# Kernel optimization log

Hardware: AMD Instinct MI355X
Metric: run time of the kernel (lower is better)

## Reference

```python
import jax, jax.numpy as jnp
import numpy as np

B, N, C, H = 2, 512, 64, 8

def setup_inputs() -> dict:
    key = jax.random.key(0)
    k1, k2, k3, k4, k5 = jax.random.split(key, 5)
    query = jax.random.normal(k1, (B, N, N, C), dtype=jnp.float32)
    key_t = jax.random.normal(k2, (B, N, N, C), dtype=jnp.float32)
    roi_mask = jax.random.uniform(k3, (B, N, N), dtype=jnp.float32)
    W = jax.random.normal(k4, (H, 2 * C), dtype=jnp.float32) * (1.0 / np.sqrt(2 * C))
    b = jax.random.normal(k5, (H,), dtype=jnp.float32) * 0.01
    return {"query": query, "key": key_t, "roi_mask": roi_mask, "W": W, "b": b}

def reference(query, key, roi_mask, W, b):
    # ft = cat(query, key) along feature dim -> [B, N, N, 2C]
    # small GEMM: scores [B, N, N, H]; split the matmul to avoid materializing concat
    Wq, Wk = W[:, :C], W[:, C:]  # [H, C] each
    attn = jnp.einsum('bmnc,hc->bmnh', query, Wq) \
         + jnp.einsum('bmnc,hc->bmnh', key, Wk) + b
    attn = jnp.exp(attn) * roi_mask[:, :, :, None]
    attn_sum = attn.sum(axis=2)  # [B, N, H]
    return attn / attn_sum[:, :, None, :]
```

## Files before the change

### kernel.cpp

```cpp
#include <hip/hip_runtime.h>
#include <math.h>

constexpr int BDIM    = 256;
constexpr int TILE    = 256;
constexpr int NDIM    = 512;
constexpr int CDIM    = 64;
constexpr int HDIM    = 8;
constexpr int CHALF   = 32;
constexpr int LSTRIDE = CHALF + 1;

__global__ __launch_bounds__(BDIM)
void mha_kernel(const float* __restrict__ q,
                const float* __restrict__ kk,
                const float* __restrict__ mask,
                const float* __restrict__ W,
                const float* __restrict__ bias,
                float* __restrict__ out)
{
    __shared__ float tile_lds[TILE * LSTRIDE];
    __shared__ float red[4 * HDIM];
    __shared__ float rsum_lds[HDIM];

    const int bm = blockIdx.x;
    const int t  = threadIdx.x;

    const float* qrow = q  + (size_t)bm * NDIM * CDIM;
    const float* krow = kk + (size_t)bm * NDIM * CDIM;

    float val[2][HDIM];
    float psum[HDIM];
#pragma unroll
    for (int h = 0; h < HDIM; ++h) psum[h] = 0.0f;

#pragma unroll
    for (int tl = 0; tl < 2; ++tl) {
        const int n0 = tl * TILE;
        float acc[HDIM];
#pragma unroll
        for (int h = 0; h < HDIM; ++h) acc[h] = 0.0f;

        for (int ph = 0; ph < 4; ++ph) {
            const float* srcbase = (ph < 2) ? qrow : krow;
            const float* src = srcbase + (size_t)n0 * CDIM + (ph & 1) * CHALF;

            __syncthreads();
#pragma unroll
            for (int i = 0; i < 8; ++i) {
                int f4 = t + i * BDIM;
                int n  = f4 >> 3;
                int c4 = (f4 & 7) << 2;
                float4 v = *(const float4*)(src + n * CDIM + c4);
                float* d = &tile_lds[n * LSTRIDE + c4];
                d[0] = v.x; d[1] = v.y; d[2] = v.z; d[3] = v.w;
            }
            __syncthreads();

            float x[CHALF];
            const float* xs = &tile_lds[t * LSTRIDE];
#pragma unroll
            for (int c = 0; c < CHALF; ++c) x[c] = xs[c];

            const float* wp = W + ph * CHALF;
#pragma unroll
            for (int h = 0; h < HDIM; ++h) {
                float a = acc[h];
#pragma unroll
                for (int c = 0; c < CHALF; ++c)
                    a = fmaf(x[c], wp[h * 2 * CDIM + c], a);
                acc[h] = a;
            }
        }

        const float mval = mask[bm * NDIM + n0 + t];
#pragma unroll
        for (int h = 0; h < HDIM; ++h) {
            float v = __expf(acc[h] + bias[h]) * mval;
            val[tl][h] = v;
            psum[h] += v;
        }
    }

#pragma unroll
    for (int h = 0; h < HDIM; ++h) {
        float s = psum[h];
#pragma unroll
        for (int off = 32; off >= 1; off >>= 1)
            s += __shfl_xor(s, off, 64);
        psum[h] = s;
    }
    const int lane = t & 63;
    const int wid  = t >> 6;
    if (lane == 0) {
#pragma unroll
        for (int h = 0; h < HDIM; ++h) red[wid * HDIM + h] = psum[h];
    }
    __syncthreads();
    if (t < HDIM) {
        float s = red[t] + red[HDIM + t] + red[2 * HDIM + t] + red[3 * HDIM + t];
        rsum_lds[t] = 1.0f / s;
    }
    __syncthreads();

    float rs[HDIM];
#pragma unroll
    for (int h = 0; h < HDIM; ++h) rs[h] = rsum_lds[h];

    float* orow = out + (size_t)bm * NDIM * HDIM;
#pragma unroll
    for (int tl = 0; tl < 2; ++tl) {
        const int n = tl * TILE + t;
        float4 lo = make_float4(val[tl][0] * rs[0], val[tl][1] * rs[1],
                                val[tl][2] * rs[2], val[tl][3] * rs[3]);
        float4 hi = make_float4(val[tl][4] * rs[4], val[tl][5] * rs[5],
                                val[tl][6] * rs[6], val[tl][7] * rs[7]);
        float4* op = (float4*)(orow + (size_t)n * HDIM);
        op[0] = lo;
        op[1] = hi;
    }
}

extern "C" void kernel_launch(void* const* d_in, const int* in_sizes, int n_in,
                              void* d_out, int out_size, void* d_ws, size_t ws_size,
                              hipStream_t stream) {
    const float* q    = (const float*)d_in[0];
    const float* k    = (const float*)d_in[1];
    const float* mask = (const float*)d_in[2];
    const float* W    = (const float*)d_in[3];
    const float* b    = (const float*)d_in[4];
    float* out = (float*)d_out;

    hipLaunchKernelGGL(mha_kernel, dim3(2 * NDIM), dim3(BDIM), 0, stream,
                       q, k, mask, W, b, out);
}
```

Before: 298.1 us.

## Load query/key rows directly into registers instead of staging through LDS

Drops the shared-memory tile staging and its barriers. Each thread now reads its own 64-float query and key rows with float4 global loads into registers and computes all eight head dot products, and launch bounds request four blocks per CU. This removes LDS traffic and syncs, but each thread's loads now stride 256 bytes apart, so global access is uncoalesced per instruction, and the 64-float register array raises register pressure.

```diff
diff --git a/kernel.cpp b/kernel.cpp
--- a/kernel.cpp
+++ b/kernel.cpp
@@ -1,15 +1,12 @@
 #include <hip/hip_runtime.h>
 #include <math.h>
 
-constexpr int BDIM    = 256;
-constexpr int TILE    = 256;
-constexpr int NDIM    = 512;
-constexpr int CDIM    = 64;
-constexpr int HDIM    = 8;
-constexpr int CHALF   = 32;
-constexpr int LSTRIDE = CHALF + 1;
+constexpr int BDIM = 256;
+constexpr int NDIM = 512;
+constexpr int CDIM = 64;
+constexpr int HDIM = 8;
 
-__global__ __launch_bounds__(BDIM)
+__global__ __launch_bounds__(BDIM, 4)
 void mha_kernel(const float* __restrict__ q,
                 const float* __restrict__ kk,
                 const float* __restrict__ mask,
@@ -17,7 +14,6 @@
                 const float* __restrict__ bias,
                 float* __restrict__ out)
 {
-    __shared__ float tile_lds[TILE * LSTRIDE];
     __shared__ float red[4 * HDIM];
     __shared__ float rsum_lds[HDIM];
 
@@ -34,44 +30,53 @@
 
 #pragma unroll
     for (int tl = 0; tl < 2; ++tl) {
-        const int n0 = tl * TILE;
+        const int n = tl * BDIM + t;
+
         float acc[HDIM];
 #pragma unroll
         for (int h = 0; h < HDIM; ++h) acc[h] = 0.0f;
 
-        for (int ph = 0; ph < 4; ++ph) {
-            const float* srcbase = (ph < 2) ? qrow : krow;
-            const float* src = srcbase + (size_t)n0 * CDIM + (ph & 1) * CHALF;
-
-            __syncthreads();
+        {
+            const float4* qp = (const float4*)(qrow + (size_t)n * CDIM);
+            float x[CDIM];
 #pragma unroll
-            for (int i = 0; i < 8; ++i) {
-                int f4 = t + i * BDIM;
-                int n  = f4 >> 3;
-                int c4 = (f4 & 7) << 2;
-                float4 v = *(const float4*)(src + n * CDIM + c4);
-                float* d = &tile_lds[n * LSTRIDE + c4];
-                d[0] = v.x; d[1] = v.y; d[2] = v.z; d[3] = v.w;
+            for (int j = 0; j < 16; ++j) {
+                float4 v = qp[j];
+                x[4 * j + 0] = v.x; x[4 * j + 1] = v.y;
+                x[4 * j + 2] = v.z; x[4 * j + 3] = v.w;
             }
-            __syncthreads();
-
-            float x[CHALF];
-            const float* xs = &tile_lds[t * LSTRIDE];
-#pragma unroll
-            for (int c = 0; c < CHALF; ++c) x[c] = xs[c];
-
-            const float* wp = W + ph * CHALF;
 #pragma unroll
             for (int h = 0; h < HDIM; ++h) {
+                const float* wq = W + h * 2 * CDIM;
                 float a = acc[h];
 #pragma unroll
-                for (int c = 0; c < CHALF; ++c)
-                    a = fmaf(x[c], wp[h * 2 * CDIM + c], a);
+                for (int c = 0; c < CDIM; ++c)
+                    a = fmaf(x[c], wq[c], a);
                 acc[h] = a;
             }
         }
 
-        const float mval = mask[bm * NDIM + n0 + t];
+        {
+            const float4* kp = (const float4*)(krow + (size_t)n * CDIM);
+            float x[CDIM];
+#pragma unroll
+            for (int j = 0; j < 16; ++j) {
+                float4 v = kp[j];
+                x[4 * j + 0] = v.x; x[4 * j + 1] = v.y;
+                x[4 * j + 2] = v.z; x[4 * j + 3] = v.w;
+            }
+#pragma unroll
+            for (int h = 0; h < HDIM; ++h) {
+                const float* wk = W + h * 2 * CDIM + CDIM;
+                float a = acc[h];
+#pragma unroll
+                for (int c = 0; c < CDIM; ++c)
+                    a = fmaf(x[c], wk[c], a);
+                acc[h] = a;
+            }
+        }
+
+        const float mval = mask[bm * NDIM + n];
 #pragma unroll
         for (int h = 0; h < HDIM; ++h) {
             float v = __expf(acc[h] + bias[h]) * mval;
@@ -108,7 +113,7 @@
     float* orow = out + (size_t)bm * NDIM * HDIM;
 #pragma unroll
     for (int tl = 0; tl < 2; ++tl) {
-        const int n = tl * TILE + t;
+        const int n = tl * BDIM + t;
         float4 lo = make_float4(val[tl][0] * rs[0], val[tl][1] * rs[1],
                                 val[tl][2] * rs[2], val[tl][3] * rs[3]);
         float4 hi = make_float4(val[tl][4] * rs[4], val[tl][5] * rs[5],
```

Result: no change. 296.6 us (-0.5%).

## Split into chunked projection kernel plus separate normalization kernel

Applied to the files above, without the earlier changes.

Each row of the work now goes to 16 blocks of 32 columns instead of one block. Each block computes the unnormalized exp scores with per-thread float4 loads and a shuffle reduction across 16 lanes, then writes partial sums to the workspace. A second kernel reads the partial sums and rescales the output in place. This removes the LDS staging and transposed reads, and gives far more blocks for parallelism and latency hiding. The cost is a second launch and an extra read and write of the output.

```diff
diff --git a/kernel.cpp b/kernel.cpp
--- a/kernel.cpp
+++ b/kernel.cpp
@@ -1,121 +1,136 @@
 #include <hip/hip_runtime.h>
 #include <math.h>
 
-constexpr int BDIM    = 256;
-constexpr int TILE    = 256;
-constexpr int NDIM    = 512;
-constexpr int CDIM    = 64;
-constexpr int HDIM    = 8;
-constexpr int CHALF   = 32;
-constexpr int LSTRIDE = CHALF + 1;
+constexpr int NDIM  = 512;
+constexpr int CDIM  = 64;
+constexpr int HDIM  = 8;
+constexpr int CHUNK = 32;
+constexpr int NCHNK = NDIM / CHUNK;
 
-__global__ __launch_bounds__(BDIM)
-void mha_kernel(const float* __restrict__ q,
-                const float* __restrict__ kk,
-                const float* __restrict__ mask,
-                const float* __restrict__ W,
-                const float* __restrict__ bias,
-                float* __restrict__ out)
+__global__ __launch_bounds__(256, 4)
+void k1_proj(const float* __restrict__ q,
+             const float* __restrict__ kk,
+             const float* __restrict__ mask,
+             const float* __restrict__ W,
+             const float* __restrict__ bias,
+             float* __restrict__ out,
+             float* __restrict__ ws_partial)
 {
-    __shared__ float tile_lds[TILE * LSTRIDE];
+    __shared__ float lds_val[CHUNK * 9];
     __shared__ float red[4 * HDIM];
-    __shared__ float rsum_lds[HDIM];
 
-    const int bm = blockIdx.x;
-    const int t  = threadIdx.x;
+    const int blk = blockIdx.x;
+    const int bm  = blk >> 4;
+    const int ch  = blk & 15;
+    const int t   = threadIdx.x;
+    const int c4  = t & 15;
+    const int sub = t >> 4;
 
-    const float* qrow = q  + (size_t)bm * NDIM * CDIM;
-    const float* krow = kk + (size_t)bm * NDIM * CDIM;
+    const float4* W4 = (const float4*)W;
+    float4 wq[HDIM], wk[HDIM];
+#pragma unroll
+    for (int h = 0; h < HDIM; ++h) {
+        wq[h] = W4[h * 32 + c4];
+        wk[h] = W4[h * 32 + 16 + c4];
+    }
+    float bz[HDIM];
+#pragma unroll
+    for (int h = 0; h < HDIM; ++h) bz[h] = bias[h];
 
-    float val[2][HDIM];
+    const size_t rowbase = ((size_t)bm * NDIM + (size_t)ch * CHUNK);
+    const float4* qbase = (const float4*)(q  + rowbase * CDIM);
+    const float4* kbase = (const float4*)(kk + rowbase * CDIM);
+
     float psum[HDIM];
 #pragma unroll
     for (int h = 0; h < HDIM; ++h) psum[h] = 0.0f;
 
 #pragma unroll
-    for (int tl = 0; tl < 2; ++tl) {
-        const int n0 = tl * TILE;
-        float acc[HDIM];
-#pragma unroll
-        for (int h = 0; h < HDIM; ++h) acc[h] = 0.0f;
+    for (int pass = 0; pass < 2; ++pass) {
+        const int rr = pass * 16 + sub;
+        const float4 xq = qbase[pass * 256 + t];
+        const float4 xk = kbase[pass * 256 + t];
+        const float mval = mask[bm * NDIM + ch * CHUNK + rr];
 
-        for (int ph = 0; ph < 4; ++ph) {
-            const float* srcbase = (ph < 2) ? qrow : krow;
-            const float* src = srcbase + (size_t)n0 * CDIM + (ph & 1) * CHALF;
-
-            __syncthreads();
-#pragma unroll
-            for (int i = 0; i < 8; ++i) {
-                int f4 = t + i * BDIM;
-                int n  = f4 >> 3;
-                int c4 = (f4 & 7) << 2;
-                float4 v = *(const float4*)(src + n * CDIM + c4);
-                float* d = &tile_lds[n * LSTRIDE + c4];
-                d[0] = v.x; d[1] = v.y; d[2] = v.z; d[3] = v.w;
-            }
-            __syncthreads();
-
-            float x[CHALF];
-            const float* xs = &tile_lds[t * LSTRIDE];
-#pragma unroll
-            for (int c = 0; c < CHALF; ++c) x[c] = xs[c];
-
-            const float* wp = W + ph * CHALF;
-#pragma unroll
-            for (int h = 0; h < HDIM; ++h) {
-                float a = acc[h];
-#pragma unroll
-                for (int c = 0; c < CHALF; ++c)
-                    a = fmaf(x[c], wp[h * 2 * CDIM + c], a);
-                acc[h] = a;
-            }
-        }
-
-        const float mval = mask[bm * NDIM + n0 + t];
 #pragma unroll
         for (int h = 0; h < HDIM; ++h) {
-            float v = __expf(acc[h] + bias[h]) * mval;
-            val[tl][h] = v;
+            float a = xq.x * wq[h].x + xq.y * wq[h].y
+                    + xq.z * wq[h].z + xq.w * wq[h].w
+                    + xk.x * wk[h].x + xk.y * wk[h].y
+                    + xk.z * wk[h].z + xk.w * wk[h].w;
+            a += __shfl_xor(a, 1, 64);
+            a += __shfl_xor(a, 2, 64);
+            a += __shfl_xor(a, 4, 64);
+            a += __shfl_xor(a, 8, 64);
+            float v = __expf(a + bz[h]) * mval;
             psum[h] += v;
+            if (c4 == 0) lds_val[rr * 9 + h] = v;
         }
     }
 
 #pragma unroll
     for (int h = 0; h < HDIM; ++h) {
         float s = psum[h];
-#pragma unroll
-        for (int off = 32; off >= 1; off >>= 1)
-            s += __shfl_xor(s, off, 64);
+        s += __shfl_xor(s, 16, 64);
+        s += __shfl_xor(s, 32, 64);
         psum[h] = s;
     }
-    const int lane = t & 63;
-    const int wid  = t >> 6;
-    if (lane == 0) {
+    if ((t & 63) == 0) {
+        const int w = t >> 6;
 #pragma unroll
-        for (int h = 0; h < HDIM; ++h) red[wid * HDIM + h] = psum[h];
-    }
-    __syncthreads();
-    if (t < HDIM) {
-        float s = red[t] + red[HDIM + t] + red[2 * HDIM + t] + red[3 * HDIM + t];
-        rsum_lds[t] = 1.0f / s;
+        for (int h = 0; h < HDIM; ++h) red[w * HDIM + h] = psum[h];
     }
     __syncthreads();
 
-    float rs[HDIM];
+    if (t < HDIM) {
+        float s = red[t] + red[HDIM + t] + red[2 * HDIM + t] + red[3 * HDIM + t];
+        ws_partial[(size_t)(bm * NCHNK + ch) * HDIM + t] = s;
+    }
+
+    if (t < 64) {
+        const int row = t >> 1;
+        const int hb  = (t & 1) * 4;
+        float4 o;
+        o.x = lds_val[row * 9 + hb + 0];
+        o.y = lds_val[row * 9 + hb + 1];
+        o.z = lds_val[row * 9 + hb + 2];
+        o.w = lds_val[row * 9 + hb + 3];
+        ((float4*)(out + rowbase * HDIM))[t] = o;
+    }
+}
+
+__global__ __launch_bounds__(256, 4)
+void k2_norm(const float* __restrict__ ws_partial,
+             float* __restrict__ out)
+{
+    __shared__ float part[NCHNK * HDIM];
+    __shared__ float rsum[HDIM];
+
+    const int bm = blockIdx.x;
+    const int t  = threadIdx.x;
+
+    if (t < NCHNK * HDIM)
+        part[t] = ws_partial[(size_t)bm * NCHNK * HDIM + t];
+    __syncthreads();
+    if (t < HDIM) {
+        float s = 0.0f;
 #pragma unroll
-    for (int h = 0; h < HDIM; ++h) rs[h] = rsum_lds[h];
+        for (int c = 0; c < NCHNK; ++c) s += part[c * HDIM + t];
+        rsum[t] = 1.0f / s;
+    }
+    __syncthreads();
 
-    float* orow = out + (size_t)bm * NDIM * HDIM;
+    float4 rs0 = make_float4(rsum[0], rsum[1], rsum[2], rsum[3]);
+    float4 rs1 = make_float4(rsum[4], rsum[5], rsum[6], rsum[7]);
+
+    float4* o4 = (float4*)(out + (size_t)bm * NDIM * HDIM);
 #pragma unroll
-    for (int tl = 0; tl < 2; ++tl) {
-        const int n = tl * TILE + t;
-        float4 lo = make_float4(val[tl][0] * rs[0], val[tl][1] * rs[1],
-                                val[tl][2] * rs[2], val[tl][3] * rs[3]);
-        float4 hi = make_float4(val[tl][4] * rs[4], val[tl][5] * rs[5],
-                                val[tl][6] * rs[6], val[tl][7] * rs[7]);
-        float4* op = (float4*)(orow + (size_t)n * HDIM);
-        op[0] = lo;
-        op[1] = hi;
+    for (int i = 0; i < 4; ++i) {
+        const int idx = i * 256 + t;
+        float4 v = o4[idx];
+        const float4 sc = (idx & 1) ? rs1 : rs0;
+        v.x *= sc.x; v.y *= sc.y; v.z *= sc.z; v.w *= sc.w;
+        o4[idx] = v;
     }
 }
 
@@ -128,7 +143,10 @@
     const float* W    = (const float*)d_in[3];
     const float* b    = (const float*)d_in[4];
     float* out = (float*)d_out;
+    float* ws_partial = (float*)d_ws;
 
-    hipLaunchKernelGGL(mha_kernel, dim3(2 * NDIM), dim3(BDIM), 0, stream,
-                       q, k, mask, W, b, out);
+    hipLaunchKernelGGL(k1_proj, dim3(2 * NDIM * NCHNK), dim3(256), 0, stream,
+                       q, k, mask, W, b, out, ws_partial);
+    hipLaunchKernelGGL(k2_norm, dim3(2 * NDIM), dim3(256), 0, stream,
+                       ws_partial, out);
 }
```

Result: no change. 299.2 us (+0.4%).
